# Kernel tuning notes

Measured on AMD Instinct MI355X. Metric: run time of the kernel, lower is better.

## Reference

```python
import jax, jax.numpy as jnp
import numpy as np

N_NODES = 50000
N_EDGES = 800000
N_FEAT = 128
N_HID = 128
N_CLASS = 40


def _mean_aggregate(x, src, dst, num_nodes):
    # PyG 'mean' aggregation: for each target node, mean of source-neighbor features.
    msgs = x[src]                                             # [E, D] gather
    sums = jax.ops.segment_sum(msgs, dst, num_segments=num_nodes)   # [N, D]
    ones = jnp.ones((src.shape[0],), dtype=x.dtype)
    cnt = jax.ops.segment_sum(ones, dst, num_segments=num_nodes)    # [N]
    return sums / jnp.maximum(cnt, 1.0)[:, None]


def setup_inputs() -> dict:
    key = jax.random.key(0)
    ks = jax.random.split(key, 8)
    x = jax.random.normal(ks[0], (N_NODES, N_FEAT), dtype=jnp.float32)
    edge_index = jax.random.randint(ks[1], (2, N_EDGES), 0, N_NODES, dtype=jnp.int64)
    s1 = 1.0 / np.sqrt(N_FEAT)
    s2 = 1.0 / np.sqrt(N_HID)
    return {
        "x": x,
        "edge_index": edge_index,
        # SAGEConv 1: lin_l acts on aggregated neighbors (has bias), lin_r on root (no bias)
        "Wl1": jax.random.normal(ks[2], (N_FEAT, N_HID), dtype=jnp.float32) * s1,
        "Wr1": jax.random.normal(ks[3], (N_FEAT, N_HID), dtype=jnp.float32) * s1,
        "b1": jnp.zeros((N_HID,), dtype=jnp.float32),
        # SAGEConv 2 (gc2)
        "Wl2": jax.random.normal(ks[4], (N_HID, N_CLASS), dtype=jnp.float32) * s2,
        "Wr2": jax.random.normal(ks[5], (N_HID, N_CLASS), dtype=jnp.float32) * s2,
        "b2": jnp.zeros((N_CLASS,), dtype=jnp.float32),
    }


def reference(x, edge_index, Wl1, Wr1, b1, Wl2, Wr2, b2):
    src, dst = edge_index[0], edge_index[1]
    n = x.shape[0]
    # Layer 1: SAGEConv -> relu (dropout is identity in eval mode)
    agg = _mean_aggregate(x, src, dst, n)                 # [N, F]
    h = jax.nn.relu(agg @ Wl1 + x @ Wr1 + b1)             # [N, H]
    # Layer 2: SAGEConv (logits)
    agg2 = _mean_aggregate(h, src, dst, n)                # [N, H]
    out = agg2 @ Wl2 + h @ Wr2 + b2                       # [N, C]
    return out
```

## Files before the change

### kernel.cpp

```cpp
#include <hip/hip_runtime.h>
#include <hip/hip_bf16.h>

#define N_FEAT 128
#define N_HID  128
#define N_CLASS 40

#define NP   256
#define PSZ  196
#define BCAP 4096
#define BCHUNK 4096

typedef __attribute__((ext_vector_type(8))) __bf16 bf16x8;
typedef __attribute__((ext_vector_type(4))) float f32x4;

__device__ __forceinline__ unsigned short f2bf(float f) {
    union { float f; unsigned int u; } v; v.f = f;
    unsigned int r = (v.u + 0x7FFFu + ((v.u >> 16) & 1u)) >> 16;
    return (unsigned short)r;
}
__device__ __forceinline__ float bf2f_lo(unsigned int p) {
    union { unsigned int u; float f; } v; v.u = p << 16; return v.f;
}
__device__ __forceinline__ float bf2f_hi(unsigned int p) {
    union { unsigned int u; float f; } v; v.u = p & 0xFFFF0000u; return v.f;
}

__global__ __launch_bounds__(256) void k_bin(const int* __restrict__ src,
                                             const int* __restrict__ dst,
                                             int* __restrict__ ptail,
                                             uint2* __restrict__ bins, int E) {
    __shared__ uint2 stage[BCHUNK];
    __shared__ int lcnt[NP], lofs[NP], lcur[NP], gbase[NP];
    __shared__ int ws4[4];
    int t = threadIdx.x;
    int base = blockIdx.x * BCHUNK;
    int nE = min(BCHUNK, E - base);
    lcnt[t] = 0;
    __syncthreads();
    for (int i = t; i < nE; i += 256) {
        int d = dst[base + i];
        atomicAdd(&lcnt[d / PSZ], 1);
    }
    __syncthreads();
    {
        int v = lcnt[t];
        int lane = t & 63, wid = t >> 6;
        int inc = v;
        #pragma unroll
        for (int s = 1; s < 64; s <<= 1) {
            int u = __shfl_up(inc, s);
            if (lane >= s) inc += u;
        }
        if (lane == 63) ws4[wid] = inc;
        __syncthreads();
        int wb = 0;
        for (int w = 0; w < wid; ++w) wb += ws4[w];
        int exc = wb + inc - v;
        lofs[t] = exc;
        lcur[t] = exc;
        gbase[t] = atomicAdd(&ptail[t], v);
    }
    __syncthreads();
    for (int i = t; i < nE; i += 256) {
        int d = dst[base + i];
        int s = src[base + i];
        int pos = atomicAdd(&lcur[d / PSZ], 1);
        stage[pos] = make_uint2((unsigned)s, (unsigned)d);
    }
    __syncthreads();
    for (int i = t; i < nE; i += 256) {
        uint2 pr = stage[i];
        int p = (int)pr.y / PSZ;
        bins[(size_t)p * BCAP + gbase[p] + (i - lofs[p])] = pr;
    }
}

__global__ __launch_bounds__(256) void k_pcount(const uint2* __restrict__ bins,
                                                const int* __restrict__ ptail,
                                                int* __restrict__ cnt, int N) {
    int p = blockIdx.x;
    __shared__ int lc[PSZ];
    int t = threadIdx.x;
    if (t < PSZ) lc[t] = 0;
    __syncthreads();
    int n = ptail[p];
    const uint2* bp = bins + (size_t)p * BCAP;
    for (int i = t; i < n; i += 256)
        atomicAdd(&lc[(int)bp[i].y - p * PSZ], 1);
    __syncthreads();
    int g = p * PSZ + t;
    if (t < PSZ && g < N) cnt[g] = lc[t];
}

__global__ __launch_bounds__(256) void k_place(const uint2* __restrict__ bins,
                                               const int* __restrict__ ptail,
                                               const int* __restrict__ off,
                                               int* __restrict__ srt, int N) {
    int p = blockIdx.x;
    __shared__ int lcur[PSZ];
    int t = threadIdx.x;
    int g = p * PSZ + t;
    if (t < PSZ) lcur[t] = (g < N) ? off[g] : 0;
    __syncthreads();
    int n = ptail[p];
    const uint2* bp = bins + (size_t)p * BCAP;
    for (int i = t; i < n; i += 256) {
        uint2 pr = bp[i];
        int pos = atomicAdd(&lcur[(int)pr.y - p * PSZ], 1);
        srt[pos] = (int)pr.x;
    }
}

__global__ __launch_bounds__(256) void k_scan1(const int* __restrict__ cnt,
                                               int* __restrict__ bsum, int n) {
    int i = blockIdx.x * 256 + threadIdx.x;
    int v = (i < n) ? cnt[i] : 0;
    #pragma unroll
    for (int s = 1; s < 64; s <<= 1) v += __shfl_xor(v, s);
    __shared__ int ws[4];
    if ((threadIdx.x & 63) == 0) ws[threadIdx.x >> 6] = v;
    __syncthreads();
    if (threadIdx.x == 0) bsum[blockIdx.x] = ws[0] + ws[1] + ws[2] + ws[3];
}

__global__ __launch_bounds__(256) void k_scan2(const int* __restrict__ bsum,
                                               int* __restrict__ bexc,
                                               int nb, int* __restrict__ off, int n) {
    int tid = threadIdx.x;
    int lane = tid & 63, wid = tid >> 6;
    int v = (tid < nb) ? bsum[tid] : 0;
    int inc = v;
    #pragma unroll
    for (int s = 1; s < 64; s <<= 1) {
        int t = __shfl_up(inc, s);
        if (lane >= s) inc += t;
    }
    __shared__ int ws[4];
    if (lane == 63) ws[wid] = inc;
    __syncthreads();
    int wbase = 0;
    for (int w = 0; w < wid; ++w) wbase += ws[w];
    int exc = wbase + inc - v;
    if (tid < nb) bexc[tid] = exc;
    if (tid == nb - 1) off[n] = exc + v;
}

__global__ __launch_bounds__(256) void k_scan3(const int* __restrict__ cnt,
                                               const int* __restrict__ bexc,
                                               int* __restrict__ off, int n) {
    int i = blockIdx.x * 256 + threadIdx.x;
    int lane = threadIdx.x & 63, wid = threadIdx.x >> 6;
    int v = (i < n) ? cnt[i] : 0;
    int inc = v;
    #pragma unroll
    for (int s = 1; s < 64; s <<= 1) {
        int t = __shfl_up(inc, s);
        if (lane >= s) inc += t;
    }
    __shared__ int ws[4];
    if (lane == 63) ws[wid] = inc;
    __syncthreads();
    int wbase = 0;
    for (int w = 0; w < wid; ++w) wbase += ws[w];
    int exc = bexc[blockIdx.x] + wbase + inc - v;
    if (i < n) off[i] = exc;
}

__global__ void k_cvt(const float* __restrict__ in, unsigned short* __restrict__ outp, int n) {
    int i = (blockIdx.x * 256 + threadIdx.x) * 4;
    if (i >= n) return;
    float4 v = *(const float4*)(in + i);
    ushort4 o;
    o.x = f2bf(v.x); o.y = f2bf(v.y); o.z = f2bf(v.z); o.w = f2bf(v.w);
    *(ushort4*)(outp + i) = o;
}

__global__ void k_swz(const float* __restrict__ W, unsigned short* __restrict__ sw,
                      int ncols, int nt) {
    int t = blockIdx.x * 256 + threadIdx.x;
    if (t >= nt * 4 * 64) return;
    int lane = t & 63;
    int bi = t >> 6;
    int kc = bi & 3, ct = bi >> 2;
    int n = lane & 15, q = lane >> 4;
    int col = ct * 16 + n;
    #pragma unroll
    for (int j = 0; j < 8; ++j) {
        int k = kc * 32 + q * 8 + j;
        float f = (col < ncols) ? W[(size_t)k * ncols + col] : 0.f;
        sw[(size_t)t * 8 + j] = f2bf(f);
    }
}

__global__ void k_swzc(const float* __restrict__ Wl2, const float* __restrict__ Wr2,
                       unsigned short* __restrict__ sw) {
    int t = blockIdx.x * 256 + threadIdx.x;
    if (t >= 5 * 4 * 64) return;
    int lane = t & 63;
    int bi = t >> 6;
    int kc = bi & 3, ct = bi >> 2;
    int n = lane & 15, q = lane >> 4;
    int col = ct * 16 + n;
    #pragma unroll
    for (int j = 0; j < 8; ++j) {
        int k = kc * 32 + q * 8 + j;
        float f = (col < N_CLASS) ? Wl2[(size_t)k * N_CLASS + col]
                                  : Wr2[(size_t)k * N_CLASS + (col - N_CLASS)];
        sw[(size_t)t * 8 + j] = f2bf(f);
    }
}

__global__ __launch_bounds__(256) void k_aggb4(const unsigned short* __restrict__ feat,
                                               const int* __restrict__ srt,
                                               const int* __restrict__ off,
                                               unsigned short* __restrict__ outp, int n_nodes) {
    int wave = (blockIdx.x * blockDim.x + threadIdx.x) >> 6;
    int lane = threadIdx.x & 63;
    if (wave >= n_nodes) return;
    int q = lane >> 4;
    int l = lane & 15;
    int beg = off[wave];
    int end = off[wave + 1];
    float a0 = 0.f, a1 = 0.f, a2 = 0.f, a3 = 0.f,
          a4 = 0.f, a5 = 0.f, a6 = 0.f, a7 = 0.f;
    int e = beg + q;
    #define ACCUM128(P) { \
        a0 += bf2f_lo(P.x); a1 += bf2f_hi(P.x); \
        a2 += bf2f_lo(P.y); a3 += bf2f_hi(P.y); \
        a4 += bf2f_lo(P.z); a5 += bf2f_hi(P.z); \
        a6 += bf2f_lo(P.w); a7 += bf2f_hi(P.w); }
    for (; e + 4 < end; e += 8) {
        int s0 = srt[e];
        int s1 = srt[e + 4];
        uint4 p0 = *(const uint4*)(feat + (size_t)s0 * N_FEAT + l * 8);
        uint4 p1 = *(const uint4*)(feat + (size_t)s1 * N_FEAT + l * 8);
        ACCUM128(p0)
        ACCUM128(p1)
    }
    if (e < end) {
        int s0 = srt[e];
        uint4 p0 = *(const uint4*)(feat + (size_t)s0 * N_FEAT + l * 8);
        ACCUM128(p0)
    }
    #undef ACCUM128
    #define RED(A) A += __shfl_xor(A, 16); A += __shfl_xor(A, 32);
    RED(a0) RED(a1) RED(a2) RED(a3) RED(a4) RED(a5) RED(a6) RED(a7)
    #undef RED
    if (q == 0) {
        int c = end - beg;
        float inv = 1.0f / (float)(c > 1 ? c : 1);
        uint4 o;
        o.x = ((unsigned int)f2bf(a1 * inv) << 16) | f2bf(a0 * inv);
        o.y = ((unsigned int)f2bf(a3 * inv) << 16) | f2bf(a2 * inv);
        o.z = ((unsigned int)f2bf(a5 * inv) << 16) | f2bf(a4 * inv);
        o.w = ((unsigned int)f2bf(a7 * inv) << 16) | f2bf(a6 * inv);
        *(uint4*)(outp + (size_t)wave * N_FEAT + l * 8) = o;
    }
}

__global__ __launch_bounds__(256) void k_agg40(const unsigned short* __restrict__ p2b,
                                               const float* __restrict__ r2,
                                               const int* __restrict__ srt,
                                               const int* __restrict__ off,
                                               float* __restrict__ outp, int n_nodes) {
    int wave = (blockIdx.x * blockDim.x + threadIdx.x) >> 6;
    int lane = threadIdx.x & 63;
    if (wave >= n_nodes) return;
    int q = lane >> 4;
    int l = lane & 15;
    int beg = off[wave];
    int end = off[wave + 1];
    float a0 = 0.f, a1 = 0.f, a2 = 0.f, a3 = 0.f;
    int e = beg + q;
    #define ACCUM64(P) { \
        a0 += bf2f_lo(P.x); a1 += bf2f_hi(P.x); \
        a2 += bf2f_lo(P.y); a3 += bf2f_hi(P.y); }
    for (; e + 4 < end; e += 8) {
        int s0 = srt[e];
        int s1 = srt[e + 4];
        uint2 p0 = *(const uint2*)(p2b + (size_t)s0 * 64 + l * 4);
        uint2 p1 = *(const uint2*)(p2b + (size_t)s1 * 64 + l * 4);
        ACCUM64(p0)
        ACCUM64(p1)
    }
    if (e < end) {
        int s0 = srt[e];
        uint2 p0 = *(const uint2*)(p2b + (size_t)s0 * 64 + l * 4);
        ACCUM64(p0)
    }
    #undef ACCUM64
    #define RED(A) A += __shfl_xor(A, 16); A += __shfl_xor(A, 32);
    RED(a0) RED(a1) RED(a2) RED(a3)
    #undef RED
    if (lane < 10) {
        int c = end - beg;
        float inv = 1.0f / (float)(c > 1 ? c : 1);
        float4 rr = *(const float4*)(r2 + (size_t)wave * N_CLASS + lane * 4);
        float4 o;
        o.x = fmaf(a0, inv, rr.x);
        o.y = fmaf(a1, inv, rr.y);
        o.z = fmaf(a2, inv, rr.z);
        o.w = fmaf(a3, inv, rr.w);
        *(float4*)(outp + (size_t)wave * N_CLASS + lane * 4) = o;
    }
}

__global__ __launch_bounds__(256) void k_gemm1m(const unsigned short* __restrict__ aggb,
                                                const unsigned short* __restrict__ xb,
                                                const unsigned short* __restrict__ Bl,
                                                const unsigned short* __restrict__ Br,
                                                const float* __restrict__ bias,
                                                unsigned short* __restrict__ hb, int n_nodes) {
    int wid = (blockIdx.x * 256 + threadIdx.x) >> 6;
    int lane = threadIdx.x & 63;
    int nb = wid * 16;
    if (nb >= n_nodes) return;
    int m = lane & 15, q = lane >> 4;
    size_t abase = (size_t)(nb + m) * N_FEAT + q * 8;
    bf16x8 Aa0 = *(const bf16x8*)(aggb + abase);
    bf16x8 Aa1 = *(const bf16x8*)(aggb + abase + 32);
    bf16x8 Aa2 = *(const bf16x8*)(aggb + abase + 64);
    bf16x8 Aa3 = *(const bf16x8*)(aggb + abase + 96);
    bf16x8 Ax0 = *(const bf16x8*)(xb + abase);
    bf16x8 Ax1 = *(const bf16x8*)(xb + abase + 32);
    bf16x8 Ax2 = *(const bf16x8*)(xb + abase + 64);
    bf16x8 Ax3 = *(const bf16x8*)(xb + abase + 96);
    const bf16x8* blp = (const bf16x8*)Bl + lane;
    const bf16x8* brp = (const bf16x8*)Br + lane;

    #pragma unroll
    for (int ct = 0; ct < 8; ++ct) {
        f32x4 acc = {0.f, 0.f, 0.f, 0.f};
        acc = __builtin_amdgcn_mfma_f32_16x16x32_bf16(Aa0, blp[(ct*4+0)*64], acc, 0,0,0);
        acc = __builtin_amdgcn_mfma_f32_16x16x32_bf16(Ax0, brp[(ct*4+0)*64], acc, 0,0,0);
        acc = __builtin_amdgcn_mfma_f32_16x16x32_bf16(Aa1, blp[(ct*4+1)*64], acc, 0,0,0);
        acc = __builtin_amdgcn_mfma_f32_16x16x32_bf16(Ax1, brp[(ct*4+1)*64], acc, 0,0,0);
        acc = __builtin_amdgcn_mfma_f32_16x16x32_bf16(Aa2, blp[(ct*4+2)*64], acc, 0,0,0);
        acc = __builtin_amdgcn_mfma_f32_16x16x32_bf16(Ax2, brp[(ct*4+2)*64], acc, 0,0,0);
        acc = __builtin_amdgcn_mfma_f32_16x16x32_bf16(Aa3, blp[(ct*4+3)*64], acc, 0,0,0);
        acc = __builtin_amdgcn_mfma_f32_16x16x32_bf16(Ax3, brp[(ct*4+3)*64], acc, 0,0,0);
        int col = ct * 16 + m;
        float bv = bias[col];
        hb[(size_t)(nb + q*4 + 0) * N_HID + col] = f2bf(fmaxf(acc.x + bv, 0.f));
        hb[(size_t)(nb + q*4 + 1) * N_HID + col] = f2bf(fmaxf(acc.y + bv, 0.f));
        hb[(size_t)(nb + q*4 + 2) * N_HID + col] = f2bf(fmaxf(acc.z + bv, 0.f));
        hb[(size_t)(nb + q*4 + 3) * N_HID + col] = f2bf(fmaxf(acc.w + bv, 0.f));
    }
}

__global__ __launch_bounds__(256) void k_gemm2p(const unsigned short* __restrict__ hb,
                                                const unsigned short* __restrict__ Bc,
                                                const float* __restrict__ bias2,
                                                unsigned short* __restrict__ p2b,
                                                float* __restrict__ r2, int n_nodes) {
    int wid = (blockIdx.x * 256 + threadIdx.x) >> 6;
    int lane = threadIdx.x & 63;
    int nb = wid * 16;
    if (nb >= n_nodes) return;
    int m = lane & 15, q = lane >> 4;
    size_t abase = (size_t)(nb + m) * N_HID + q * 8;
    bf16x8 Ah0 = *(const bf16x8*)(hb + abase);
    bf16x8 Ah1 = *(const bf16x8*)(hb + abase + 32);
    bf16x8 Ah2 = *(const bf16x8*)(hb + abase + 64);
    bf16x8 Ah3 = *(const bf16x8*)(hb + abase + 96);
    const bf16x8* bcp = (const bf16x8*)Bc + lane;

    #pragma unroll
    for (int ct = 0; ct < 5; ++ct) {
        f32x4 acc = {0.f, 0.f, 0.f, 0.f};
        acc = __builtin_amdgcn_mfma_f32_16x16x32_bf16(Ah0, bcp[(ct*4+0)*64], acc, 0,0,0);
        acc = __builtin_amdgcn_mfma_f32_16x16x32_bf16(Ah1, bcp[(ct*4+1)*64], acc, 0,0,0);
        acc = __builtin_amdgcn_mfma_f32_16x16x32_bf16(Ah2, bcp[(ct*4+2)*64], acc, 0,0,0);
        acc = __builtin_amdgcn_mfma_f32_16x16x32_bf16(Ah3, bcp[(ct*4+3)*64], acc, 0,0,0);
        int col = ct * 16 + m;
        if (col < N_CLASS) {
            p2b[(size_t)(nb + q*4 + 0) * 64 + col] = f2bf(acc.x);
            p2b[(size_t)(nb + q*4 + 1) * 64 + col] = f2bf(acc.y);
            p2b[(size_t)(nb + q*4 + 2) * 64 + col] = f2bf(acc.z);
            p2b[(size_t)(nb + q*4 + 3) * 64 + col] = f2bf(acc.w);
        } else {
            int rc = col - N_CLASS;
            float bv = bias2[rc];
            r2[(size_t)(nb + q*4 + 0) * N_CLASS + rc] = acc.x + bv;
            r2[(size_t)(nb + q*4 + 1) * N_CLASS + rc] = acc.y + bv;
            r2[(size_t)(nb + q*4 + 2) * N_CLASS + rc] = acc.z + bv;
            r2[(size_t)(nb + q*4 + 3) * N_CLASS + rc] = acc.w + bv;
        }
    }
}

extern "C" void kernel_launch(void* const* d_in, const int* in_sizes, int n_in,
                              void* d_out, int out_size, void* d_ws, size_t ws_size,
                              hipStream_t stream) {
    const float* x   = (const float*)d_in[0];
    const int*   ei  = (const int*)d_in[1];
    const float* Wl1 = (const float*)d_in[2];
    const float* Wr1 = (const float*)d_in[3];
    const float* b1  = (const float*)d_in[4];
    const float* Wl2 = (const float*)d_in[5];
    const float* Wr2 = (const float*)d_in[6];
    const float* b2  = (const float*)d_in[7];
    float* out = (float*)d_out;

    const int N = in_sizes[0] / N_FEAT;
    const int E = in_sizes[1] / 2;
    const int* src = ei;
    const int* dst = ei + E;

    unsigned short* xb   = (unsigned short*)d_ws;
    unsigned short* aggb = xb + (size_t)N * N_FEAT;
    unsigned short* hb   = aggb + (size_t)N * N_FEAT;
    unsigned short* p2b  = hb + (size_t)N * N_HID;
    float* r2 = (float*)(p2b + (size_t)N * 64);
    uint2* bins = (uint2*)p2b;
    unsigned short* w1l  = (unsigned short*)(r2 + (size_t)N * N_CLASS);
    unsigned short* w1r  = w1l + 16384;
    unsigned short* wc   = w1r + 16384;
    int* cnt = (int*)(wc + 10240);
    cnt = (int*)(((uintptr_t)cnt + 15) & ~(uintptr_t)15);
    int* off = cnt + N;
    int* srt = off + N + 1;
    int* ptail = srt + E;
    int* bsum = ptail + NP;
    int* bexc = bsum + 256;

    hipMemsetAsync(ptail, 0, NP * sizeof(int), stream);

    const int TB = 256;
    int sblocks = (N + TB - 1) / TB;
    int bblocks = (E + BCHUNK - 1) / BCHUNK;

    k_cvt<<<((N * N_FEAT / 4) + TB - 1) / TB, TB, 0, stream>>>(x, xb, N * N_FEAT);
    k_swz<<<(8 * 4 * 64 + TB - 1) / TB, TB, 0, stream>>>(Wl1, w1l, N_HID, 8);
    k_swz<<<(8 * 4 * 64 + TB - 1) / TB, TB, 0, stream>>>(Wr1, w1r, N_HID, 8);
    k_swzc<<<(5 * 4 * 64 + TB - 1) / TB, TB, 0, stream>>>(Wl2, Wr2, wc);

    k_bin<<<bblocks, TB, 0, stream>>>(src, dst, ptail, bins, E);
    k_pcount<<<NP, TB, 0, stream>>>(bins, ptail, cnt, N);
    k_scan1<<<sblocks, TB, 0, stream>>>(cnt, bsum, N);
    k_scan2<<<1, TB, 0, stream>>>(bsum, bexc, sblocks, off, N);
    k_scan3<<<sblocks, TB, 0, stream>>>(cnt, bexc, off, N);
    k_place<<<NP, TB, 0, stream>>>(bins, ptail, off, srt, N);

    int aggblocks = (N * 64 + TB - 1) / TB;
    int gblocks = ((N + 15) / 16 + 3) / 4;

    k_aggb4<<<aggblocks, TB, 0, stream>>>(xb, srt, off, aggb, N);
    k_gemm1m<<<gblocks, TB, 0, stream>>>(aggb, xb, w1l, w1r, b1, hb, N);

    k_gemm2p<<<gblocks, TB, 0, stream>>>(hb, wc, b2, p2b, r2, N);
    k_agg40<<<aggblocks, TB, 0, stream>>>(p2b, r2, srt, off, out, N);
}
```

Before: 222.0 us.

## Fuse prep kernels, collapse CSR scan pipeline, and fuse both GEMMs via LDS

Merges the x conversion, the weight swizzles and the ptail zeroing into one prep kernel, which replaces a memset and four launches. Replaces the count, three-stage scan and place kernels with a 256-entry partition scan plus one build kernel that does the local count, scan, offset write and placement. Fuses the layer-1 and layer-2 GEMMs by keeping each wave's h tile in padded LDS, so h is never written to or read from global memory. Shrinks the p2b row stride from 64 to 40 bf16, which cuts gather bytes in the final aggregation but leaves 8-byte loads only 8-byte aligned.

```diff
diff --git a/kernel.cpp b/kernel.cpp
--- a/kernel.cpp
+++ b/kernel.cpp
@@ -10,6 +10,8 @@
 #define BCAP 4096
 #define BCHUNK 4096
 
+#define HSTRIDE 136
+
 typedef __attribute__((ext_vector_type(8))) __bf16 bf16x8;
 typedef __attribute__((ext_vector_type(4))) float f32x4;
 
@@ -23,6 +25,70 @@
 }
 __device__ __forceinline__ float bf2f_hi(unsigned int p) {
     union { unsigned int u; float f; } v; v.u = p & 0xFFFF0000u; return v.f;
+}
+
+__device__ __forceinline__ void swz_body(const float* __restrict__ W,
+                                         unsigned short* __restrict__ sw,
+                                         int ncols, int t, int nt) {
+    if (t >= nt * 4 * 64) return;
+    int lane = t & 63;
+    int bi = t >> 6;
+    int kc = bi & 3, ct = bi >> 2;
+    int n = lane & 15, q = lane >> 4;
+    int col = ct * 16 + n;
+    #pragma unroll
+    for (int j = 0; j < 8; ++j) {
+        int k = kc * 32 + q * 8 + j;
+        float f = (col < ncols) ? W[(size_t)k * ncols + col] : 0.f;
+        sw[(size_t)t * 8 + j] = f2bf(f);
+    }
+}
+__device__ __forceinline__ void swzc_body(const float* __restrict__ Wl2,
+                                          const float* __restrict__ Wr2,
+                                          unsigned short* __restrict__ sw, int t) {
+    if (t >= 5 * 4 * 64) return;
+    int lane = t & 63;
+    int bi = t >> 6;
+    int kc = bi & 3, ct = bi >> 2;
+    int n = lane & 15, q = lane >> 4;
+    int col = ct * 16 + n;
+    #pragma unroll
+    for (int j = 0; j < 8; ++j) {
+        int k = kc * 32 + q * 8 + j;
+        float f = (col < N_CLASS) ? Wl2[(size_t)k * N_CLASS + col]
+                                  : Wr2[(size_t)k * N_CLASS + (col - N_CLASS)];
+        sw[(size_t)t * 8 + j] = f2bf(f);
+    }
+}
+
+__global__ __launch_bounds__(256) void k_prep(const float* __restrict__ x,
+                                              unsigned short* __restrict__ xb, int nCvt, int nElem,
+                                              const float* __restrict__ Wl1,
+                                              const float* __restrict__ Wr1,
+                                              const float* __restrict__ Wl2,
+                                              const float* __restrict__ Wr2,
+                                              unsigned short* __restrict__ w1l,
+                                              unsigned short* __restrict__ w1r,
+                                              unsigned short* __restrict__ wc,
+                                              int* __restrict__ ptail) {
+    int b = blockIdx.x, t = threadIdx.x;
+    if (b < nCvt) {
+        int i = (b * 256 + t) * 4;
+        if (i < nElem) {
+            float4 v = *(const float4*)(x + i);
+            ushort4 o;
+            o.x = f2bf(v.x); o.y = f2bf(v.y); o.z = f2bf(v.z); o.w = f2bf(v.w);
+            *(ushort4*)(xb + i) = o;
+        }
+        return;
+    }
+    b -= nCvt;
+    if (b < 8) { swz_body(Wl1, w1l, N_HID, b * 256 + t, 8); return; }
+    b -= 8;
+    if (b < 8) { swz_body(Wr1, w1r, N_HID, b * 256 + t, 8); return; }
+    b -= 8;
+    if (b < 5) { swzc_body(Wl2, Wr2, wc, b * 256 + t); return; }
+    ptail[t] = 0;
 }
 
 __global__ __launch_bounds__(256) void k_bin(const int* __restrict__ src,
@@ -75,138 +141,66 @@
     }
 }
 
-__global__ __launch_bounds__(256) void k_pcount(const uint2* __restrict__ bins,
-                                                const int* __restrict__ ptail,
-                                                int* __restrict__ cnt, int N) {
+__global__ __launch_bounds__(256) void k_pscan(const int* __restrict__ ptail,
+                                               int* __restrict__ pbase,
+                                               int* __restrict__ off, int N) {
+    int t = threadIdx.x;
+    int lane = t & 63, wid = t >> 6;
+    int v = ptail[t];
+    int inc = v;
+    #pragma unroll
+    for (int s = 1; s < 64; s <<= 1) {
+        int u = __shfl_up(inc, s);
+        if (lane >= s) inc += u;
+    }
+    __shared__ int ws[4];
+    if (lane == 63) ws[wid] = inc;
+    __syncthreads();
+    int wb = 0;
+    for (int w = 0; w < wid; ++w) wb += ws[w];
+    pbase[t] = wb + inc - v;
+    if (t == NP - 1) off[N] = wb + inc;
+}
+
+__global__ __launch_bounds__(256) void k_build(const uint2* __restrict__ bins,
+                                               const int* __restrict__ ptail,
+                                               const int* __restrict__ pbase,
+                                               int* __restrict__ off,
+                                               int* __restrict__ srt, int N) {
     int p = blockIdx.x;
-    __shared__ int lc[PSZ];
+    __shared__ int lc[256], lofs[256];
+    __shared__ int ws4[4];
     int t = threadIdx.x;
-    if (t < PSZ) lc[t] = 0;
+    lc[t] = 0;
     __syncthreads();
     int n = ptail[p];
     const uint2* bp = bins + (size_t)p * BCAP;
     for (int i = t; i < n; i += 256)
         atomicAdd(&lc[(int)bp[i].y - p * PSZ], 1);
     __syncthreads();
+    {
+        int v = lc[t];
+        int lane = t & 63, wid = t >> 6;
+        int inc = v;
+        #pragma unroll
+        for (int s = 1; s < 64; s <<= 1) {
+            int u = __shfl_up(inc, s);
+            if (lane >= s) inc += u;
+        }
+        if (lane == 63) ws4[wid] = inc;
+        __syncthreads();
+        int wb = 0;
+        for (int w = 0; w < wid; ++w) wb += ws4[w];
+        lofs[t] = pbase[p] + wb + inc - v;
+    }
+    __syncthreads();
     int g = p * PSZ + t;
-    if (t < PSZ && g < N) cnt[g] = lc[t];
-}
-
-__global__ __launch_bounds__(256) void k_place(const uint2* __restrict__ bins,
-                                               const int* __restrict__ ptail,
-                                               const int* __restrict__ off,
-                                               int* __restrict__ srt, int N) {
-    int p = blockIdx.x;
-    __shared__ int lcur[PSZ];
-    int t = threadIdx.x;
-    int g = p * PSZ + t;
-    if (t < PSZ) lcur[t] = (g < N) ? off[g] : 0;
-    __syncthreads();
-    int n = ptail[p];
-    const uint2* bp = bins + (size_t)p * BCAP;
+    if (t < PSZ && g < N) off[g] = lofs[t];
+    __syncthreads();
     for (int i = t; i < n; i += 256) {
         uint2 pr = bp[i];
-        int pos = atomicAdd(&lcur[(int)pr.y - p * PSZ], 1);
+        int pos = atomicAdd(&lofs[(int)pr.y - p * PSZ], 1);
         srt[pos] = (int)pr.x;
-    }
-}
-
-__global__ __launch_bounds__(256) void k_scan1(const int* __restrict__ cnt,
-                                               int* __restrict__ bsum, int n) {
-    int i = blockIdx.x * 256 + threadIdx.x;
-    int v = (i < n) ? cnt[i] : 0;
-    #pragma unroll
-    for (int s = 1; s < 64; s <<= 1) v += __shfl_xor(v, s);
-    __shared__ int ws[4];
-    if ((threadIdx.x & 63) == 0) ws[threadIdx.x >> 6] = v;
-    __syncthreads();
-    if (threadIdx.x == 0) bsum[blockIdx.x] = ws[0] + ws[1] + ws[2] + ws[3];
-}
-
-__global__ __launch_bounds__(256) void k_scan2(const int* __restrict__ bsum,
-                                               int* __restrict__ bexc,
-                                               int nb, int* __restrict__ off, int n) {
-    int tid = threadIdx.x;
-    int lane = tid & 63, wid = tid >> 6;
-    int v = (tid < nb) ? bsum[tid] : 0;
-    int inc = v;
-    #pragma unroll
-    for (int s = 1; s < 64; s <<= 1) {
-        int t = __shfl_up(inc, s);
-        if (lane >= s) inc += t;
-    }
-    __shared__ int ws[4];
-    if (lane == 63) ws[wid] = inc;
-    __syncthreads();
-    int wbase = 0;
-    for (int w = 0; w < wid; ++w) wbase += ws[w];
-    int exc = wbase + inc - v;
-    if (tid < nb) bexc[tid] = exc;
-    if (tid == nb - 1) off[n] = exc + v;
-}
-
-__global__ __launch_bounds__(256) void k_scan3(const int* __restrict__ cnt,
-                                               const int* __restrict__ bexc,
-                                               int* __restrict__ off, int n) {
-    int i = blockIdx.x * 256 + threadIdx.x;
-    int lane = threadIdx.x & 63, wid = threadIdx.x >> 6;
-    int v = (i < n) ? cnt[i] : 0;
-    int inc = v;
-    #pragma unroll
-    for (int s = 1; s < 64; s <<= 1) {
-        int t = __shfl_up(inc, s);
-        if (lane >= s) inc += t;
-    }
-    __shared__ int ws[4];
-    if (lane == 63) ws[wid] = inc;
-    __syncthreads();
-    int wbase = 0;
-    for (int w = 0; w < wid; ++w) wbase += ws[w];
-    int exc = bexc[blockIdx.x] + wbase + inc - v;
-    if (i < n) off[i] = exc;
-}
-
-__global__ void k_cvt(const float* __restrict__ in, unsigned short* __restrict__ outp, int n) {
-    int i = (blockIdx.x * 256 + threadIdx.x) * 4;
-    if (i >= n) return;
-    float4 v = *(const float4*)(in + i);
-    ushort4 o;
-    o.x = f2bf(v.x); o.y = f2bf(v.y); o.z = f2bf(v.z); o.w = f2bf(v.w);
-    *(ushort4*)(outp + i) = o;
-}
-
-__global__ void k_swz(const float* __restrict__ W, unsigned short* __restrict__ sw,
-                      int ncols, int nt) {
-    int t = blockIdx.x * 256 + threadIdx.x;
-    if (t >= nt * 4 * 64) return;
-    int lane = t & 63;
-    int bi = t >> 6;
-    int kc = bi & 3, ct = bi >> 2;
-    int n = lane & 15, q = lane >> 4;
-    int col = ct * 16 + n;
-    #pragma unroll
-    for (int j = 0; j < 8; ++j) {
-        int k = kc * 32 + q * 8 + j;
-        float f = (col < ncols) ? W[(size_t)k * ncols + col] : 0.f;
-        sw[(size_t)t * 8 + j] = f2bf(f);
-    }
-}
-
-__global__ void k_swzc(const float* __restrict__ Wl2, const float* __restrict__ Wr2,
-                       unsigned short* __restrict__ sw) {
-    int t = blockIdx.x * 256 + threadIdx.x;
-    if (t >= 5 * 4 * 64) return;
-    int lane = t & 63;
-    int bi = t >> 6;
-    int kc = bi & 3, ct = bi >> 2;
-    int n = lane & 15, q = lane >> 4;
-    int col = ct * 16 + n;
-    #pragma unroll
-    for (int j = 0; j < 8; ++j) {
-        int k = kc * 32 + q * 8 + j;
-        float f = (col < N_CLASS) ? Wl2[(size_t)k * N_CLASS + col]
-                                  : Wr2[(size_t)k * N_CLASS + (col - N_CLASS)];
-        sw[(size_t)t * 8 + j] = f2bf(f);
     }
 }
 
@@ -258,61 +252,20 @@
     }
 }
 
-__global__ __launch_bounds__(256) void k_agg40(const unsigned short* __restrict__ p2b,
-                                               const float* __restrict__ r2,
-                                               const int* __restrict__ srt,
-                                               const int* __restrict__ off,
-                                               float* __restrict__ outp, int n_nodes) {
-    int wave = (blockIdx.x * blockDim.x + threadIdx.x) >> 6;
-    int lane = threadIdx.x & 63;
-    if (wave >= n_nodes) return;
-    int q = lane >> 4;
-    int l = lane & 15;
-    int beg = off[wave];
-    int end = off[wave + 1];
-    float a0 = 0.f, a1 = 0.f, a2 = 0.f, a3 = 0.f;
-    int e = beg + q;
-    #define ACCUM64(P) { \
-        a0 += bf2f_lo(P.x); a1 += bf2f_hi(P.x); \
-        a2 += bf2f_lo(P.y); a3 += bf2f_hi(P.y); }
-    for (; e + 4 < end; e += 8) {
-        int s0 = srt[e];
-        int s1 = srt[e + 4];
-        uint2 p0 = *(const uint2*)(p2b + (size_t)s0 * 64 + l * 4);
-        uint2 p1 = *(const uint2*)(p2b + (size_t)s1 * 64 + l * 4);
-        ACCUM64(p0)
-        ACCUM64(p1)
-    }
-    if (e < end) {
-        int s0 = srt[e];
-        uint2 p0 = *(const uint2*)(p2b + (size_t)s0 * 64 + l * 4);
-        ACCUM64(p0)
-    }
-    #undef ACCUM64
-    #define RED(A) A += __shfl_xor(A, 16); A += __shfl_xor(A, 32);
-    RED(a0) RED(a1) RED(a2) RED(a3)
-    #undef RED
-    if (lane < 10) {
-        int c = end - beg;
-        float inv = 1.0f / (float)(c > 1 ? c : 1);
-        float4 rr = *(const float4*)(r2 + (size_t)wave * N_CLASS + lane * 4);
-        float4 o;
-        o.x = fmaf(a0, inv, rr.x);
-        o.y = fmaf(a1, inv, rr.y);
-        o.z = fmaf(a2, inv, rr.z);
-        o.w = fmaf(a3, inv, rr.w);
-        *(float4*)(outp + (size_t)wave * N_CLASS + lane * 4) = o;
-    }
-}
-
-__global__ __launch_bounds__(256) void k_gemm1m(const unsigned short* __restrict__ aggb,
+__global__ __launch_bounds__(256) void k_gemm12(const unsigned short* __restrict__ aggb,
                                                 const unsigned short* __restrict__ xb,
                                                 const unsigned short* __restrict__ Bl,
                                                 const unsigned short* __restrict__ Br,
-                                                const float* __restrict__ bias,
-                                                unsigned short* __restrict__ hb, int n_nodes) {
-    int wid = (blockIdx.x * 256 + threadIdx.x) >> 6;
-    int lane = threadIdx.x & 63;
+                                                const float* __restrict__ bias1,
+                                                const unsigned short* __restrict__ Bc,
+                                                const float* __restrict__ bias2,
+                                                unsigned short* __restrict__ p2b,
+                                                float* __restrict__ r2, int n_nodes) {
+    __shared__ unsigned short hlds[4][16 * HSTRIDE];
+    int tid = threadIdx.x;
+    int wv = tid >> 6;
+    int wid = (blockIdx.x * 256 + tid) >> 6;
+    int lane = tid & 63;
     int nb = wid * 16;
     if (nb >= n_nodes) return;
     int m = lane & 15, q = lane >> 4;
@@ -327,6 +280,7 @@
     bf16x8 Ax3 = *(const bf16x8*)(xb + abase + 96);
     const bf16x8* blp = (const bf16x8*)Bl + lane;
     const bf16x8* brp = (const bf16x8*)Br + lane;
+    unsigned short* hl = hlds[wv];
 
     #pragma unroll
     for (int ct = 0; ct < 8; ++ct) {
@@ -340,44 +294,31 @@
         acc = __builtin_amdgcn_mfma_f32_16x16x32_bf16(Aa3, blp[(ct*4+3)*64], acc, 0,0,0);
         acc = __builtin_amdgcn_mfma_f32_16x16x32_bf16(Ax3, brp[(ct*4+3)*64], acc, 0,0,0);
         int col = ct * 16 + m;
-        float bv = bias[col];
-        hb[(size_t)(nb + q*4 + 0) * N_HID + col] = f2bf(fmaxf(acc.x + bv, 0.f));
-        hb[(size_t)(nb + q*4 + 1) * N_HID + col] = f2bf(fmaxf(acc.y + bv, 0.f));
-        hb[(size_t)(nb + q*4 + 2) * N_HID + col] = f2bf(fmaxf(acc.z + bv, 0.f));
-        hb[(size_t)(nb + q*4 + 3) * N_HID + col] = f2bf(fmaxf(acc.w + bv, 0.f));
-    }
-}
-
-__global__ __launch_bounds__(256) void k_gemm2p(const unsigned short* __restrict__ hb,
-                                                const unsigned short* __restrict__ Bc,
-                                                const float* __restrict__ bias2,
-                                                unsigned short* __restrict__ p2b,
-                                                float* __restrict__ r2, int n_nodes) {
-    int wid = (blockIdx.x * 256 + threadIdx.x) >> 6;
-    int lane = threadIdx.x & 63;
-    int nb = wid * 16;
-    if (nb >= n_nodes) return;
-    int m = lane & 15, q = lane >> 4;
-    size_t abase = (size_t)(nb + m) * N_HID + q * 8;
-    bf16x8 Ah0 = *(const bf16x8*)(hb + abase);
-    bf16x8 Ah1 = *(const bf16x8*)(hb + abase + 32);
-    bf16x8 Ah2 = *(const bf16x8*)(hb + abase + 64);
-    bf16x8 Ah3 = *(const bf16x8*)(hb + abase + 96);
+        float bv = bias1[col];
+        hl[(q*4 + 0) * HSTRIDE + col] = f2bf(fmaxf(acc.x + bv, 0.f));
+        hl[(q*4 + 1) * HSTRIDE + col] = f2bf(fmaxf(acc.y + bv, 0.f));
+        hl[(q*4 + 2) * HSTRIDE + col] = f2bf(fmaxf(acc.z + bv, 0.f));
+        hl[(q*4 + 3) * HSTRIDE + col] = f2bf(fmaxf(acc.w + bv, 0.f));
+    }
+    bf16x8 H0 = *(const bf16x8*)(hl + m * HSTRIDE + q * 8);
+    bf16x8 H1 = *(const bf16x8*)(hl + m * HSTRIDE + q * 8 + 32);
+    bf16x8 H2 = *(const bf16x8*)(hl + m * HSTRIDE + q * 8 + 64);
+    bf16x8 H3 = *(const bf16x8*)(hl + m * HSTRIDE + q * 8 + 96);
     const bf16x8* bcp = (const bf16x8*)Bc + lane;
 
     #pragma unroll
     for (int ct = 0; ct < 5; ++ct) {
         f32x4 acc = {0.f, 0.f, 0.f, 0.f};
-        acc = __builtin_amdgcn_mfma_f32_16x16x32_bf16(Ah0, bcp[(ct*4+0)*64], acc, 0,0,0);
-        acc = __builtin_amdgcn_mfma_f32_16x16x32_bf16(Ah1, bcp[(ct*4+1)*64], acc, 0,0,0);
-        acc = __builtin_amdgcn_mfma_f32_16x16x32_bf16(Ah2, bcp[(ct*4+2)*64], acc, 0,0,0);
-        acc = __builtin_amdgcn_mfma_f32_16x16x32_bf16(Ah3, bcp[(ct*4+3)*64], acc, 0,0,0);
+        acc = __builtin_amdgcn_mfma_f32_16x16x32_bf16(H0, bcp[(ct*4+0)*64], acc, 0,0,0);
+        acc = __builtin_amdgcn_mfma_f32_16x16x32_bf16(H1, bcp[(ct*4+1)*64], acc, 0,0,0);
+        acc = __builtin_amdgcn_mfma_f32_16x16x32_bf16(H2, bcp[(ct*4+2)*64], acc, 0,0,0);
+        acc = __builtin_amdgcn_mfma_f32_16x16x32_bf16(H3, bcp[(ct*4+3)*64], acc, 0,0,0);
         int col = ct * 16 + m;
         if (col < N_CLASS) {
-            p2b[(size_t)(nb + q*4 + 0) * 64 + col] = f2bf(acc.x);
-            p2b[(size_t)(nb + q*4 + 1) * 64 + col] = f2bf(acc.y);
-            p2b[(size_t)(nb + q*4 + 2) * 64 + col] = f2bf(acc.z);
-            p2b[(size_t)(nb + q*4 + 3) * 64 + col] = f2bf(acc.w);
+            p2b[(size_t)(nb + q*4 + 0) * N_CLASS + col] = f2bf(acc.x);
+            p2b[(size_t)(nb + q*4 + 1) * N_CLASS + col] = f2bf(acc.y);
+            p2b[(size_t)(nb + q*4 + 2) * N_CLASS + col] = f2bf(acc.z);
+            p2b[(size_t)(nb + q*4 + 3) * N_CLASS + col] = f2bf(acc.w);
         } else {
             int rc = col - N_CLASS;
             float bv = bias2[rc];
@@ -386,6 +327,56 @@
             r2[(size_t)(nb + q*4 + 2) * N_CLASS + rc] = acc.z + bv;
             r2[(size_t)(nb + q*4 + 3) * N_CLASS + rc] = acc.w + bv;
         }
+    }
+}
+
+__global__ __launch_bounds__(256) void k_agg40(const unsigned short* __restrict__ p2b,
+                                               const float* __restrict__ r2,
+                                               const int* __restrict__ srt,
+                                               const int* __restrict__ off,
+                                               float* __restrict__ outp, int n_nodes) {
+    int wave = (blockIdx.x * blockDim.x + threadIdx.x) >> 6;
+    int lane = threadIdx.x & 63;
+    if (wave >= n_nodes) return;
+    int q = lane >> 4;
+    int l = lane & 15;
+    bool act = l < 10;
+    int beg = off[wave];
+    int end = off[wave + 1];
+    float a0 = 0.f, a1 = 0.f, a2 = 0.f, a3 = 0.f;
+    int e = beg + q;
+    #define ACCUM40(P) { \
+        a0 += bf2f_lo(P.x); a1 += bf2f_hi(P.x); \
+        a2 += bf2f_lo(P.y); a3 += bf2f_hi(P.y); }
+    for (; e + 4 < end; e += 8) {
+        int s0 = srt[e];
+        int s1 = srt[e + 4];
+        if (act) {
+            uint2 p0 = *(const uint2*)(p2b + (size_t)s0 * N_CLASS + l * 4);
+            uint2 p1 = *(const uint2*)(p2b + (size_t)s1 * N_CLASS + l * 4);
+            ACCUM40(p0)
+            ACCUM40(p1)
+        }
+    }
+    if (e < end && act) {
+        int s0 = srt[e];
+        uint2 p0 = *(const uint2*)(p2b + (size_t)s0 * N_CLASS + l * 4);
+        ACCUM40(p0)
+    }
+    #undef ACCUM40
+    #define RED(A) A += __shfl_xor(A, 16); A += __shfl_xor(A, 32);
+    RED(a0) RED(a1) RED(a2) RED(a3)
+    #undef RED
+    if (lane < 10) {
+        int c = end - beg;
+        float inv = 1.0f / (float)(c > 1 ? c : 1);
+        float4 rr = *(const float4*)(r2 + (size_t)wave * N_CLASS + lane * 4);
+        float4 o;
+        o.x = fmaf(a0, inv, rr.x);
+        o.y = fmaf(a1, inv, rr.y);
+        o.z = fmaf(a2, inv, rr.z);
+        o.w = fmaf(a3, inv, rr.w);
+        *(float4*)(outp + (size_t)wave * N_CLASS + lane * 4) = o;
     }
 }
 
@@ -409,45 +400,32 @@
 
     unsigned short* xb   = (unsigned short*)d_ws;
     unsigned short* aggb = xb + (size_t)N * N_FEAT;
-    unsigned short* hb   = aggb + (size_t)N * N_FEAT;
-    unsigned short* p2b  = hb + (size_t)N * N_HID;
-    float* r2 = (float*)(p2b + (size_t)N * 64);
+    unsigned short* p2b  = aggb + (size_t)N * N_FEAT;
+    float* r2 = (float*)(p2b + (size_t)N * N_CLASS);
     uint2* bins = (uint2*)p2b;
     unsigned short* w1l  = (unsigned short*)(r2 + (size_t)N * N_CLASS);
     unsigned short* w1r  = w1l + 16384;
     unsigned short* wc   = w1r + 16384;
-    int* cnt = (int*)(wc + 10240);
-    cnt = (int*)(((uintptr_t)cnt + 15) & ~(uintptr_t)15);
-    int* off = cnt + N;
+    int* off = (int*)(wc + 10240);
     int* srt = off + N + 1;
     int* ptail = srt + E;
-    int* bsum = ptail + NP;
-    int* bexc = bsum + 256;
-
-    hipMemsetAsync(ptail, 0, NP * sizeof(int), stream);
+    int* pbase = ptail + NP;
 
     const int TB = 256;
-    int sblocks = (N + TB - 1) / TB;
+    int nCvt = (N * N_FEAT / 4 + TB - 1) / TB;
     int bblocks = (E + BCHUNK - 1) / BCHUNK;
 
-    k_cvt<<<((N * N_FEAT / 4) + TB - 1) / TB, TB, 0, stream>>>(x, xb, N * N_FEAT);
-    k_swz<<<(8 * 4 * 64 + TB - 1) / TB, TB, 0, stream>>>(Wl1, w1l, N_HID, 8);
-    k_swz<<<(8 * 4 * 64 + TB - 1) / TB, TB, 0, stream>>>(Wr1, w1r, N_HID, 8);
-    k_swzc<<<(5 * 4 * 64 + TB - 1) / TB, TB, 0, stream>>>(Wl2, Wr2, wc);
-
+    k_prep<<<nCvt + 8 + 8 + 5 + 1, TB, 0, stream>>>(x, xb, nCvt, N * N_FEAT,
+                                                    Wl1, Wr1, Wl2, Wr2,
+                                                    w1l, w1r, wc, ptail);
     k_bin<<<bblocks, TB, 0, stream>>>(src, dst, ptail, bins, E);
-    k_pcount<<<NP, TB, 0, stream>>>(bins, ptail, cnt, N);
-    k_scan1<<<sblocks, TB, 0, stream>>>(cnt, bsum, N);
-    k_scan2<<<1, TB, 0, stream>>>(bsum, bexc, sblocks, off, N);
-    k_scan3<<<sblocks, TB, 0, stream>>>(cnt, bexc, off, N);
-    k_place<<<NP, TB, 0, stream>>>(bins, ptail, off, srt, N);
+    k_pscan<<<1, TB, 0, stream>>>(ptail, pbase, off, N);
+    k_build<<<NP, TB, 0, stream>>>(bins, ptail, pbase, off, srt, N);
 
     int aggblocks = (N * 64 + TB - 1) / TB;
     int gblocks = ((N + 15) / 16 + 3) / 4;
 
     k_aggb4<<<aggblocks, TB, 0, stream>>>(xb, srt, off, aggb, N);
-    k_gemm1m<<<gblocks, TB, 0, stream>>>(aggb, xb, w1l, w1r, b1, hb, N);
-
-    k_gemm2p<<<gblocks, TB, 0, stream>>>(hb, wc, b2, p2b, r2, N);
+    k_gemm12<<<gblocks, TB, 0, stream>>>(aggb, xb, w1l, w1r, b1, wc, b2, p2b, r2, N);
     k_agg40<<<aggblocks, TB, 0, stream>>>(p2b, r2, srt, off, out, N);
 }
```

Result: faster. 189.5 us (-14.7%).
